# Kernel tuning notes

Hardware: AMD Instinct MI355X
Metric: run time of the kernel (lower is better)

## Reference

```python
import jax, jax.numpy as jnp
import numpy as np

K = 8  # args.k


def setup_inputs() -> dict:
    key = jax.random.key(0)
    k1, k2, k3 = jax.random.split(key, 3)
    b, n_pre, n_cur = 1, 8192, 16384
    pre_xyzs = jax.random.normal(k1, (b, 3, n_pre), dtype=jnp.float32)
    cur_xyzs = jax.random.normal(k2, (b, 3, n_cur), dtype=jnp.float32)
    # UpsampleNumLayer output range: sigmoid * (max_upsample_num - 1) + 1  in [1, 8]
    upsample_num = jax.random.uniform(k3, (b, n_pre), dtype=jnp.float32) * 7.0 + 1.0
    return {"pre_xyzs": pre_xyzs, "cur_xyzs": cur_xyzs, "upsample_num": upsample_num}


def _sqdist(a, b):
    # a: (b, n, 3), b: (b, m, 3) -> (b, n, m) squared euclidean distances
    return ((a * a).sum(-1)[:, :, None]
            + (b * b).sum(-1)[:, None, :]
            - 2.0 * jnp.einsum('bnc,bmc->bnm', a, b))


def reference(pre_xyzs, cur_xyzs, upsample_num):
    # pre_xyzs: (b, 3, n_pre); cur_xyzs: (b, 3, n_cur); upsample_num: (b, n_pre)
    pre_t = pre_xyzs.transpose(0, 2, 1)  # (b, n_pre, 3)
    cur_t = cur_xyzs.transpose(0, 2, 1)  # (b, n_cur, 3)

    # knnquery_heap(1, pre, cur): nearest pre index for each cur point -> (b, n_cur)
    cur2pre = jnp.argmin(_sqdist(cur_t, pre_t), axis=-1)

    # knnquery_heap(K, cur, pre): K nearest cur indices for each pre point -> (b, n_pre, K)
    _, knn_idx = jax.lax.top_k(-_sqdist(pre_t, cur_t), K)

    # real_center: gather cur2pre at knn_idx -> (b, n_pre, K)
    real_center = jax.vmap(lambda c2p, idx: c2p[idx])(cur2pre, knn_idx)
    expect_center = jnp.arange(pre_xyzs.shape[2])[None, :, None]  # (1, n_pre, 1)
    mask = (expect_center == real_center).astype(pre_xyzs.dtype)  # (b, n_pre, K)

    # knn_xyzs: gather cur_xyzs columns at knn_idx -> (b, 3, n_pre, K)
    knn_xyzs = jax.vmap(lambda pts, idx: pts[:, idx])(cur_xyzs, knn_idx)

    diff = knn_xyzs - pre_xyzs[..., None]              # (b, 3, n_pre, K)
    dist = jnp.sqrt((diff * diff).sum(axis=1))         # (b, n_pre, K), L2 over channel dim
    mean_distance = (dist * mask).sum(axis=-1) / upsample_num  # (b, n_pre)
    return mean_distance
```

## Files before the change

kernel.cpp:

```cpp
#include <hip/hip_runtime.h>

#define N_PRE 8192
#define N_CUR 16384
#define KNN   8


#define MAPPED_INF 0xFF800000u

__device__ __forceinline__ unsigned key_of(float d) {
    unsigned b = __float_as_uint(d);
    return b ^ (0x80000000u | (unsigned)((int)b >> 31));
}
__device__ __forceinline__ float float_of_key(unsigned k) {
    unsigned b = (k & 0x80000000u) ? (k ^ 0x80000000u) : ~k;
    return __uint_as_float(b);
}
__device__ __forceinline__ unsigned shfl_u32(unsigned x, int src) {
    return (unsigned)__shfl((int)x, src);
}
__device__ __forceinline__ unsigned shfl_up1_u32(unsigned x) {
    return (unsigned)__shfl_up((int)x, 1);
}

__global__ __launch_bounds__(256) void prep_kernel(
        const float* __restrict__ pre, const float* __restrict__ cur,
        float4* __restrict__ pre4, float4* __restrict__ cur4) {
    int i = blockIdx.x * 256 + threadIdx.x;
    if (i < N_CUR) {
        float x = cur[i], y = cur[N_CUR + i], z = cur[2 * N_CUR + i];
        cur4[i] = make_float4(x, y, z, fmaf(x, x, fmaf(y, y, z * z)));
    }
    if (i < N_PRE) {
        float x = pre[i], y = pre[N_PRE + i], z = pre[2 * N_PRE + i];
        pre4[i] = make_float4(-2.f * x, -2.f * y, -2.f * z,
                              fmaf(x, x, fmaf(y, y, z * z)));
    }
}

#define TILE_A 2048

__global__ __launch_bounds__(1024) void cur2pre_kernel(
        const float4* __restrict__ pre4, const float4* __restrict__ cur4,
        unsigned* __restrict__ c2p) {
    __shared__ float4 sp[TILE_A];
    const int tid  = threadIdx.x;
    const int lane = tid & 63;
    const int w    = tid >> 6;
    const int j0   = blockIdx.x * 64 + w * 4;

    const float4 c0 = cur4[j0 + 0];
    const float4 c1 = cur4[j0 + 1];
    const float4 c2 = cur4[j0 + 2];
    const float4 c3 = cur4[j0 + 3];

    const float INF = __int_as_float(0x7F800000);
    float b0 = INF, b1 = INF, b2 = INF, b3 = INF;
    int   i0 = 0,   i1 = 0,   i2 = 0,   i3 = 0;

    for (int tile = 0; tile < N_PRE; tile += TILE_A) {
        __syncthreads();
        for (int k = tid; k < TILE_A; k += 1024) sp[k] = pre4[tile + k];
        __syncthreads();

#pragma unroll 4
        for (int s = 0; s < TILE_A; s += 64) {
            float4 q = sp[s + lane];
            int idx = tile + s + lane;
            float d0 = fmaf(q.x, c0.x, fmaf(q.y, c0.y, fmaf(q.z, c0.z, q.w)));
            float d1 = fmaf(q.x, c1.x, fmaf(q.y, c1.y, fmaf(q.z, c1.z, q.w)));
            float d2 = fmaf(q.x, c2.x, fmaf(q.y, c2.y, fmaf(q.z, c2.z, q.w)));
            float d3 = fmaf(q.x, c3.x, fmaf(q.y, c3.y, fmaf(q.z, c3.z, q.w)));
            if (d0 < b0) { b0 = d0; i0 = idx; }
            if (d1 < b1) { b1 = d1; i1 = idx; }
            if (d2 < b2) { b2 = d2; i2 = idx; }
            if (d3 < b3) { b3 = d3; i3 = idx; }
        }
    }

    float        bs[4] = {b0, b1, b2, b3};
    int          is[4] = {i0, i1, i2, i3};
#pragma unroll
    for (int t = 0; t < 4; ++t) {
        unsigned long long v =
            (((unsigned long long)key_of(bs[t])) << 32) | (unsigned)is[t];
#pragma unroll
        for (int off = 32; off > 0; off >>= 1) {
            unsigned long long o = __shfl_xor((unsigned long long)v, off);
            v = (o < v) ? o : v;
        }
        if (lane == 0) c2p[j0 + t] = (unsigned)(v & 0xFFFFFFFFull);
    }
}

#define TILE_B 2048

__global__ __launch_bounds__(1024) void knn_finalize_kernel(
        const float4* __restrict__ pre4, const float4* __restrict__ cur4,
        const float* __restrict__ ups,
        const unsigned* __restrict__ c2p,
        float* __restrict__ out) {
    __shared__ float4 sc[TILE_B];
    const int tid  = threadIdx.x;
    const int lane = tid & 63;
    const int w    = tid >> 6;
    const int i0   = blockIdx.x * 32 + w * 2;
    const int i1   = i0 + 1;

    const float4 p0 = pre4[i0];
    const float4 p1 = pre4[i1];

    unsigned ld0 = MAPPED_INF, li0 = 0u;
    unsigned ld1 = MAPPED_INF, li1 = 0u;
    float t80 = __int_as_float(0x7F800000);
    float t81 = t80;

    for (int tile = 0; tile < N_CUR; tile += TILE_B) {
        __syncthreads();
        for (int k = tid; k < TILE_B; k += 1024) sc[k] = cur4[tile + k];
        __syncthreads();

#pragma unroll 4
        for (int s = 0; s < TILE_B; s += 64) {
            float4 c = sc[s + lane];
            float d0 = fmaf(p0.x, c.x, fmaf(p0.y, c.y, fmaf(p0.z, c.z, c.w)));
            float d1 = fmaf(p1.x, c.x, fmaf(p1.y, c.y, fmaf(p1.z, c.z, c.w)));
            int jj = tile + s + lane;

            unsigned long long m0 = __ballot(d0 < t80);
            while (m0) {
                int src = __ffsll(m0) - 1;
                float fd = __uint_as_float(shfl_u32(__float_as_uint(d0), src));
                unsigned kd = key_of(fd);
                unsigned kj = shfl_u32((unsigned)jj, src);
                unsigned ud = shfl_up1_u32(ld0);
                unsigned uj = shfl_up1_u32(li0);
                if (lane == 0) ud = 0u;
                bool hi = kd < ud, lo = kd < ld0;
                ld0 = hi ? ud : (lo ? kd : ld0);
                li0 = hi ? uj : (lo ? kj : li0);
                t80 = float_of_key(shfl_u32(ld0, 7));
                m0 = (m0 & (m0 - 1)) & __ballot(d0 < t80);
            }

            unsigned long long m1 = __ballot(d1 < t81);
            while (m1) {
                int src = __ffsll(m1) - 1;
                float fd = __uint_as_float(shfl_u32(__float_as_uint(d1), src));
                unsigned kd = key_of(fd);
                unsigned kj = shfl_u32((unsigned)jj, src);
                unsigned ud = shfl_up1_u32(ld1);
                unsigned uj = shfl_up1_u32(li1);
                if (lane == 0) ud = 0u;
                bool hi = kd < ud, lo = kd < ld1;
                ld1 = hi ? ud : (lo ? kd : ld1);
                li1 = hi ? uj : (lo ? kj : li1);
                t81 = float_of_key(shfl_u32(ld1, 7));
                m1 = (m1 & (m1 - 1)) & __ballot(d1 < t81);
            }
        }
    }

    unsigned ja = shfl_u32(li0, lane & 7);
    unsigned jb = shfl_u32(li1, lane & 7);
    unsigned j  = (lane < 8) ? ja : jb;

    float contrib = 0.f;
    if (lane < 16) {
        float4 c = cur4[j];
        float px = -0.5f * ((lane < 8) ? p0.x : p1.x);
        float py = -0.5f * ((lane < 8) ? p0.y : p1.y);
        float pz = -0.5f * ((lane < 8) ? p0.z : p1.z);
        float dx = c.x - px, dy = c.y - py, dz = c.z - pz;
        float dsq = fmaf(dx, dx, fmaf(dy, dy, dz * dz));
        unsigned owner = c2p[j];
        unsigned iexp  = (lane < 8) ? (unsigned)i0 : (unsigned)i1;
        contrib = (owner == iexp) ? sqrtf(dsq) : 0.f;
    }
    contrib += __shfl_xor(contrib, 1);
    contrib += __shfl_xor(contrib, 2);
    contrib += __shfl_xor(contrib, 4);
    if (lane == 0) out[i0] = contrib / ups[i0];
    if (lane == 8) out[i1] = contrib / ups[i1];
}

extern "C" void kernel_launch(void* const* d_in, const int* in_sizes, int n_in,
                              void* d_out, int out_size, void* d_ws, size_t ws_size,
                              hipStream_t stream) {
    const float* pre = (const float*)d_in[0];
    const float* cur = (const float*)d_in[1];
    const float* ups = (const float*)d_in[2];
    float* out = (float*)d_out;

    char* ws = (char*)d_ws;
    unsigned* c2p = (unsigned*)ws;
    float4*   pre4 = (float4*)(ws + 65536);
    float4*   cur4 = (float4*)(ws + 65536 + 131072);

    prep_kernel<<<N_CUR / 256, 256, 0, stream>>>(pre, cur, pre4, cur4);

    cur2pre_kernel<<<N_CUR / 64, 1024, 0, stream>>>(pre4, cur4, c2p);

    knn_finalize_kernel<<<N_PRE / 32, 1024, 0, stream>>>(pre4, cur4, ups, c2p, out);
}
```

Measured before the change: 142.8 us.

## Shrink blocks and register-tile more queries per wave in both KNN kernels

Both distance kernels move from 1024-thread to 256-thread blocks. The KNN kernel now keeps four pre points per wave instead of two and loads four candidates per lane per step, so each shared-memory float4 load feeds more distance computations. A wave-wide early-out (__any over per-lane minima against the current thresholds) skips the ballot/insert loops when no candidate can enter any of the four heaps. Smaller blocks mean each block restages the whole point set through shared memory, so global and LDS staging traffic grows; register pressure also rises.

```diff
diff --git a/kernel.cpp b/kernel.cpp
--- a/kernel.cpp
+++ b/kernel.cpp
@@ -39,62 +39,65 @@
 
 #define TILE_A 2048
 
-__global__ __launch_bounds__(1024) void cur2pre_kernel(
+__global__ __launch_bounds__(256, 4) void cur2pre_kernel(
         const float4* __restrict__ pre4, const float4* __restrict__ cur4,
         unsigned* __restrict__ c2p) {
     __shared__ float4 sp[TILE_A];
     const int tid  = threadIdx.x;
     const int lane = tid & 63;
     const int w    = tid >> 6;
-    const int j0   = blockIdx.x * 64 + w * 4;
-
-    const float4 c0 = cur4[j0 + 0];
-    const float4 c1 = cur4[j0 + 1];
-    const float4 c2 = cur4[j0 + 2];
-    const float4 c3 = cur4[j0 + 3];
-
-    const float INF = __int_as_float(0x7F800000);
-    float b0 = INF, b1 = INF, b2 = INF, b3 = INF;
-    int   i0 = 0,   i1 = 0,   i2 = 0,   i3 = 0;
+    const int j0   = blockIdx.x * 16 + w * 4;
+
+    float4 cq[4];
+#pragma unroll
+    for (int q = 0; q < 4; ++q) cq[q] = cur4[j0 + q];
+
+    float    bq[4];
+    unsigned biq[4];
+#pragma unroll
+    for (int q = 0; q < 4; ++q) { bq[q] = __int_as_float(0x7F800000); biq[q] = 0u; }
 
     for (int tile = 0; tile < N_PRE; tile += TILE_A) {
         __syncthreads();
-        for (int k = tid; k < TILE_A; k += 1024) sp[k] = pre4[tile + k];
-        __syncthreads();
-
-#pragma unroll 4
-        for (int s = 0; s < TILE_A; s += 64) {
-            float4 q = sp[s + lane];
-            int idx = tile + s + lane;
-            float d0 = fmaf(q.x, c0.x, fmaf(q.y, c0.y, fmaf(q.z, c0.z, q.w)));
-            float d1 = fmaf(q.x, c1.x, fmaf(q.y, c1.y, fmaf(q.z, c1.z, q.w)));
-            float d2 = fmaf(q.x, c2.x, fmaf(q.y, c2.y, fmaf(q.z, c2.z, q.w)));
-            float d3 = fmaf(q.x, c3.x, fmaf(q.y, c3.y, fmaf(q.z, c3.z, q.w)));
-            if (d0 < b0) { b0 = d0; i0 = idx; }
-            if (d1 < b1) { b1 = d1; i1 = idx; }
-            if (d2 < b2) { b2 = d2; i2 = idx; }
-            if (d3 < b3) { b3 = d3; i3 = idx; }
+        for (int k = tid; k < TILE_A; k += 256) sp[k] = pre4[tile + k];
+        __syncthreads();
+
+        for (int s = 0; s < TILE_A; s += 256) {
+            float4 c0 = sp[s +       lane];
+            float4 c1 = sp[s +  64 + lane];
+            float4 c2 = sp[s + 128 + lane];
+            float4 c3 = sp[s + 192 + lane];
+            unsigned base = (unsigned)(tile + s + lane);
+#pragma unroll
+            for (int q = 0; q < 4; ++q) {
+                float d0 = fmaf(c0.x, cq[q].x, fmaf(c0.y, cq[q].y, fmaf(c0.z, cq[q].z, c0.w)));
+                float d1 = fmaf(c1.x, cq[q].x, fmaf(c1.y, cq[q].y, fmaf(c1.z, cq[q].z, c1.w)));
+                float d2 = fmaf(c2.x, cq[q].x, fmaf(c2.y, cq[q].y, fmaf(c2.z, cq[q].z, c2.w)));
+                float d3 = fmaf(c3.x, cq[q].x, fmaf(c3.y, cq[q].y, fmaf(c3.z, cq[q].z, c3.w)));
+                if (d0 < bq[q]) { bq[q] = d0; biq[q] = base; }
+                if (d1 < bq[q]) { bq[q] = d1; biq[q] = base + 64; }
+                if (d2 < bq[q]) { bq[q] = d2; biq[q] = base + 128; }
+                if (d3 < bq[q]) { bq[q] = d3; biq[q] = base + 192; }
+            }
         }
     }
 
-    float        bs[4] = {b0, b1, b2, b3};
-    int          is[4] = {i0, i1, i2, i3};
-#pragma unroll
-    for (int t = 0; t < 4; ++t) {
+#pragma unroll
+    for (int q = 0; q < 4; ++q) {
         unsigned long long v =
-            (((unsigned long long)key_of(bs[t])) << 32) | (unsigned)is[t];
+            (((unsigned long long)key_of(bq[q])) << 32) | biq[q];
 #pragma unroll
         for (int off = 32; off > 0; off >>= 1) {
             unsigned long long o = __shfl_xor((unsigned long long)v, off);
             v = (o < v) ? o : v;
         }
-        if (lane == 0) c2p[j0 + t] = (unsigned)(v & 0xFFFFFFFFull);
+        if (lane == 0) c2p[j0 + q] = (unsigned)(v & 0xFFFFFFFFull);
     }
 }
 
 #define TILE_B 2048
 
-__global__ __launch_bounds__(1024) void knn_finalize_kernel(
+__global__ __launch_bounds__(256, 2) void knn_finalize_kernel(
         const float4* __restrict__ pre4, const float4* __restrict__ cur4,
         const float* __restrict__ ups,
         const unsigned* __restrict__ c2p,
@@ -103,84 +106,90 @@
     const int tid  = threadIdx.x;
     const int lane = tid & 63;
     const int w    = tid >> 6;
-    const int i0   = blockIdx.x * 32 + w * 2;
-    const int i1   = i0 + 1;
-
-    const float4 p0 = pre4[i0];
-    const float4 p1 = pre4[i1];
-
-    unsigned ld0 = MAPPED_INF, li0 = 0u;
-    unsigned ld1 = MAPPED_INF, li1 = 0u;
-    float t80 = __int_as_float(0x7F800000);
-    float t81 = t80;
+    const int i0   = blockIdx.x * 16 + w * 4;
+
+    float4 pq[4];
+#pragma unroll
+    for (int t = 0; t < 4; ++t) pq[t] = pre4[i0 + t];
+
+    unsigned ld[4], li[4];
+    float    t8[4];
+#pragma unroll
+    for (int t = 0; t < 4; ++t) {
+        ld[t] = MAPPED_INF; li[t] = 0u; t8[t] = __int_as_float(0x7F800000);
+    }
 
     for (int tile = 0; tile < N_CUR; tile += TILE_B) {
         __syncthreads();
-        for (int k = tid; k < TILE_B; k += 1024) sc[k] = cur4[tile + k];
-        __syncthreads();
-
-#pragma unroll 4
-        for (int s = 0; s < TILE_B; s += 64) {
-            float4 c = sc[s + lane];
-            float d0 = fmaf(p0.x, c.x, fmaf(p0.y, c.y, fmaf(p0.z, c.z, c.w)));
-            float d1 = fmaf(p1.x, c.x, fmaf(p1.y, c.y, fmaf(p1.z, c.z, c.w)));
-            int jj = tile + s + lane;
-
-            unsigned long long m0 = __ballot(d0 < t80);
-            while (m0) {
-                int src = __ffsll(m0) - 1;
-                float fd = __uint_as_float(shfl_u32(__float_as_uint(d0), src));
-                unsigned kd = key_of(fd);
-                unsigned kj = shfl_u32((unsigned)jj, src);
-                unsigned ud = shfl_up1_u32(ld0);
-                unsigned uj = shfl_up1_u32(li0);
-                if (lane == 0) ud = 0u;
-                bool hi = kd < ud, lo = kd < ld0;
-                ld0 = hi ? ud : (lo ? kd : ld0);
-                li0 = hi ? uj : (lo ? kj : li0);
-                t80 = float_of_key(shfl_u32(ld0, 7));
-                m0 = (m0 & (m0 - 1)) & __ballot(d0 < t80);
-            }
-
-            unsigned long long m1 = __ballot(d1 < t81);
-            while (m1) {
-                int src = __ffsll(m1) - 1;
-                float fd = __uint_as_float(shfl_u32(__float_as_uint(d1), src));
-                unsigned kd = key_of(fd);
-                unsigned kj = shfl_u32((unsigned)jj, src);
-                unsigned ud = shfl_up1_u32(ld1);
-                unsigned uj = shfl_up1_u32(li1);
-                if (lane == 0) ud = 0u;
-                bool hi = kd < ud, lo = kd < ld1;
-                ld1 = hi ? ud : (lo ? kd : ld1);
-                li1 = hi ? uj : (lo ? kj : li1);
-                t81 = float_of_key(shfl_u32(ld1, 7));
-                m1 = (m1 & (m1 - 1)) & __ballot(d1 < t81);
+        for (int k = tid; k < TILE_B; k += 256) sc[k] = cur4[tile + k];
+        __syncthreads();
+
+        for (int s = 0; s < TILE_B; s += 256) {
+            float4 c0 = sc[s +       lane];
+            float4 c1 = sc[s +  64 + lane];
+            float4 c2 = sc[s + 128 + lane];
+            float4 c3 = sc[s + 192 + lane];
+            float d[4][4];
+#pragma unroll
+            for (int t = 0; t < 4; ++t) {
+                d[t][0] = fmaf(pq[t].x, c0.x, fmaf(pq[t].y, c0.y, fmaf(pq[t].z, c0.z, c0.w)));
+                d[t][1] = fmaf(pq[t].x, c1.x, fmaf(pq[t].y, c1.y, fmaf(pq[t].z, c1.z, c1.w)));
+                d[t][2] = fmaf(pq[t].x, c2.x, fmaf(pq[t].y, c2.y, fmaf(pq[t].z, c2.z, c2.w)));
+                d[t][3] = fmaf(pq[t].x, c3.x, fmaf(pq[t].y, c3.y, fmaf(pq[t].z, c3.z, c3.w)));
+            }
+            bool ev = false;
+#pragma unroll
+            for (int t = 0; t < 4; ++t) {
+                float dm = fminf(fminf(d[t][0], d[t][1]), fminf(d[t][2], d[t][3]));
+                ev = ev || (dm < t8[t]);
+            }
+            if (__any(ev)) {
+                int base = tile + s;
+#pragma unroll
+                for (int t = 0; t < 4; ++t) {
+#pragma unroll
+                    for (int k = 0; k < 4; ++k) {
+                        unsigned long long m = __ballot(d[t][k] < t8[t]);
+                        while (m) {
+                            int src = __ffsll((long long)m) - 1;
+                            float fd = __uint_as_float(
+                                shfl_u32(__float_as_uint(d[t][k]), src));
+                            unsigned kd = key_of(fd);
+                            unsigned kj = (unsigned)(base + 64 * k + src);
+                            unsigned ud = shfl_up1_u32(ld[t]);
+                            unsigned uj = shfl_up1_u32(li[t]);
+                            if (lane == 0) ud = 0u;
+                            bool hi = kd < ud, lo = kd < ld[t];
+                            ld[t] = hi ? ud : (lo ? kd : ld[t]);
+                            li[t] = hi ? uj : (lo ? kj : li[t]);
+                            t8[t] = float_of_key(shfl_u32(ld[t], 7));
+                            m = (m & (m - 1)) & __ballot(d[t][k] < t8[t]);
+                        }
+                    }
+                }
             }
         }
     }
 
-    unsigned ja = shfl_u32(li0, lane & 7);
-    unsigned jb = shfl_u32(li1, lane & 7);
-    unsigned j  = (lane < 8) ? ja : jb;
+    unsigned jt[4];
+#pragma unroll
+    for (int t = 0; t < 4; ++t) jt[t] = shfl_u32(li[t], lane & 7);
+    const int g = lane >> 3;
+    unsigned j = (g == 0) ? jt[0] : (g == 1) ? jt[1] : (g == 2) ? jt[2] : jt[3];
 
     float contrib = 0.f;
-    if (lane < 16) {
+    if (lane < 32) {
         float4 c = cur4[j];
-        float px = -0.5f * ((lane < 8) ? p0.x : p1.x);
-        float py = -0.5f * ((lane < 8) ? p0.y : p1.y);
-        float pz = -0.5f * ((lane < 8) ? p0.z : p1.z);
+        float4 p = (g == 0) ? pq[0] : (g == 1) ? pq[1] : (g == 2) ? pq[2] : pq[3];
+        float px = -0.5f * p.x, py = -0.5f * p.y, pz = -0.5f * p.z;
         float dx = c.x - px, dy = c.y - py, dz = c.z - pz;
         float dsq = fmaf(dx, dx, fmaf(dy, dy, dz * dz));
-        unsigned owner = c2p[j];
-        unsigned iexp  = (lane < 8) ? (unsigned)i0 : (unsigned)i1;
-        contrib = (owner == iexp) ? sqrtf(dsq) : 0.f;
+        contrib = (c2p[j] == (unsigned)(i0 + g)) ? sqrtf(dsq) : 0.f;
     }
     contrib += __shfl_xor(contrib, 1);
     contrib += __shfl_xor(contrib, 2);
     contrib += __shfl_xor(contrib, 4);
-    if (lane == 0) out[i0] = contrib / ups[i0];
-    if (lane == 8) out[i1] = contrib / ups[i1];
+    if (lane < 32 && (lane & 7) == 0) out[i0 + g] = contrib / ups[i0 + g];
 }
 
 extern "C" void kernel_launch(void* const* d_in, const int* in_sizes, int n_in,
@@ -192,13 +201,13 @@
     float* out = (float*)d_out;
 
     char* ws = (char*)d_ws;
-    unsigned* c2p = (unsigned*)ws;
+    unsigned* c2p  = (unsigned*)ws;
     float4*   pre4 = (float4*)(ws + 65536);
     float4*   cur4 = (float4*)(ws + 65536 + 131072);
 
     prep_kernel<<<N_CUR / 256, 256, 0, stream>>>(pre, cur, pre4, cur4);
 
-    cur2pre_kernel<<<N_CUR / 64, 1024, 0, stream>>>(pre4, cur4, c2p);
-
-    knn_finalize_kernel<<<N_PRE / 32, 1024, 0, stream>>>(pre4, cur4, ups, c2p, out);
-}
+    cur2pre_kernel<<<N_CUR / 16, 256, 0, stream>>>(pre4, cur4, c2p);
+
+    knn_finalize_kernel<<<N_PRE / 16, 256, 0, stream>>>(pre4, cur4, ups, c2p, out);
+}
```

New measurement: 163.4 us. 14.5% more time.

## Use wave-uniform ballot thresholds in argmin and batch candidate checks in kNN

Applied to the files above, without the earlier changes.

The cur2pre argmin now keeps one wave-wide best value per query. It uses a ballot against that threshold to skip iterations where no lane improves, and runs a 64-lane shuffle reduction only when some lane does. The kNN kernel processes two 64-point chunks per iteration and computes four ballots up front, so the common no-candidate case costs a single branch. Candidate indices are derived from the ballot bit instead of an extra shuffle. The trade-off is extra shuffle reductions early in the scan, when the thresholds are still loose, and the loss of the explicit unroll pragma.

```diff
diff --git a/kernel.cpp b/kernel.cpp
--- a/kernel.cpp
+++ b/kernel.cpp
@@ -54,41 +54,77 @@
     const float4 c3 = cur4[j0 + 3];
 
     const float INF = __int_as_float(0x7F800000);
-    float b0 = INF, b1 = INF, b2 = INF, b3 = INF;
-    int   i0 = 0,   i1 = 0,   i2 = 0,   i3 = 0;
+    float t0 = INF, t1 = INF, t2 = INF, t3 = INF;
+    unsigned long long bv0 = ~0ull, bv1 = ~0ull, bv2 = ~0ull, bv3 = ~0ull;
 
     for (int tile = 0; tile < N_PRE; tile += TILE_A) {
         __syncthreads();
         for (int k = tid; k < TILE_A; k += 1024) sp[k] = pre4[tile + k];
         __syncthreads();
 
-#pragma unroll 4
         for (int s = 0; s < TILE_A; s += 64) {
-            float4 q = sp[s + lane];
-            int idx = tile + s + lane;
-            float d0 = fmaf(q.x, c0.x, fmaf(q.y, c0.y, fmaf(q.z, c0.z, q.w)));
-            float d1 = fmaf(q.x, c1.x, fmaf(q.y, c1.y, fmaf(q.z, c1.z, q.w)));
-            float d2 = fmaf(q.x, c2.x, fmaf(q.y, c2.y, fmaf(q.z, c2.z, q.w)));
-            float d3 = fmaf(q.x, c3.x, fmaf(q.y, c3.y, fmaf(q.z, c3.z, q.w)));
-            if (d0 < b0) { b0 = d0; i0 = idx; }
-            if (d1 < b1) { b1 = d1; i1 = idx; }
-            if (d2 < b2) { b2 = d2; i2 = idx; }
-            if (d3 < b3) { b3 = d3; i3 = idx; }
+            float4 p = sp[s + lane];
+            unsigned idx = (unsigned)(tile + s + lane);
+            float d0 = fmaf(p.x, c0.x, fmaf(p.y, c0.y, fmaf(p.z, c0.z, p.w)));
+            float d1 = fmaf(p.x, c1.x, fmaf(p.y, c1.y, fmaf(p.z, c1.z, p.w)));
+            float d2 = fmaf(p.x, c2.x, fmaf(p.y, c2.y, fmaf(p.z, c2.z, p.w)));
+            float d3 = fmaf(p.x, c3.x, fmaf(p.y, c3.y, fmaf(p.z, c3.z, p.w)));
+
+            unsigned long long m0 = __ballot(d0 < t0);
+            unsigned long long m1 = __ballot(d1 < t1);
+            unsigned long long m2 = __ballot(d2 < t2);
+            unsigned long long m3 = __ballot(d3 < t3);
+
+            if (m0 | m1 | m2 | m3) {
+                if (m0) {
+                    unsigned long long v =
+                        (((unsigned long long)key_of(d0)) << 32) | idx;
+#pragma unroll
+                    for (int off = 32; off > 0; off >>= 1) {
+                        unsigned long long o = __shfl_xor((unsigned long long)v, off);
+                        v = (o < v) ? o : v;
+                    }
+                    if (v < bv0) { bv0 = v; t0 = float_of_key((unsigned)(bv0 >> 32)); }
+                }
+                if (m1) {
+                    unsigned long long v =
+                        (((unsigned long long)key_of(d1)) << 32) | idx;
+#pragma unroll
+                    for (int off = 32; off > 0; off >>= 1) {
+                        unsigned long long o = __shfl_xor((unsigned long long)v, off);
+                        v = (o < v) ? o : v;
+                    }
+                    if (v < bv1) { bv1 = v; t1 = float_of_key((unsigned)(bv1 >> 32)); }
+                }
+                if (m2) {
+                    unsigned long long v =
+                        (((unsigned long long)key_of(d2)) << 32) | idx;
+#pragma unroll
+                    for (int off = 32; off > 0; off >>= 1) {
+                        unsigned long long o = __shfl_xor((unsigned long long)v, off);
+                        v = (o < v) ? o : v;
+                    }
+                    if (v < bv2) { bv2 = v; t2 = float_of_key((unsigned)(bv2 >> 32)); }
+                }
+                if (m3) {
+                    unsigned long long v =
+                        (((unsigned long long)key_of(d3)) << 32) | idx;
+#pragma unroll
+                    for (int off = 32; off > 0; off >>= 1) {
+                        unsigned long long o = __shfl_xor((unsigned long long)v, off);
+                        v = (o < v) ? o : v;
+                    }
+                    if (v < bv3) { bv3 = v; t3 = float_of_key((unsigned)(bv3 >> 32)); }
+                }
+            }
         }
     }
 
-    float        bs[4] = {b0, b1, b2, b3};
-    int          is[4] = {i0, i1, i2, i3};
-#pragma unroll
-    for (int t = 0; t < 4; ++t) {
-        unsigned long long v =
-            (((unsigned long long)key_of(bs[t])) << 32) | (unsigned)is[t];
-#pragma unroll
-        for (int off = 32; off > 0; off >>= 1) {
-            unsigned long long o = __shfl_xor((unsigned long long)v, off);
-            v = (o < v) ? o : v;
-        }
-        if (lane == 0) c2p[j0 + t] = (unsigned)(v & 0xFFFFFFFFull);
+    if (lane == 0) {
+        c2p[j0 + 0] = (unsigned)(bv0 & 0xFFFFFFFFull);
+        c2p[j0 + 1] = (unsigned)(bv1 & 0xFFFFFFFFull);
+        c2p[j0 + 2] = (unsigned)(bv2 & 0xFFFFFFFFull);
+        c2p[j0 + 3] = (unsigned)(bv3 & 0xFFFFFFFFull);
     }
 }
 
@@ -119,43 +155,77 @@
         for (int k = tid; k < TILE_B; k += 1024) sc[k] = cur4[tile + k];
         __syncthreads();
 
-#pragma unroll 4
-        for (int s = 0; s < TILE_B; s += 64) {
-            float4 c = sc[s + lane];
-            float d0 = fmaf(p0.x, c.x, fmaf(p0.y, c.y, fmaf(p0.z, c.z, c.w)));
-            float d1 = fmaf(p1.x, c.x, fmaf(p1.y, c.y, fmaf(p1.z, c.z, c.w)));
-            int jj = tile + s + lane;
-
-            unsigned long long m0 = __ballot(d0 < t80);
-            while (m0) {
-                int src = __ffsll(m0) - 1;
-                float fd = __uint_as_float(shfl_u32(__float_as_uint(d0), src));
-                unsigned kd = key_of(fd);
-                unsigned kj = shfl_u32((unsigned)jj, src);
-                unsigned ud = shfl_up1_u32(ld0);
-                unsigned uj = shfl_up1_u32(li0);
-                if (lane == 0) ud = 0u;
-                bool hi = kd < ud, lo = kd < ld0;
-                ld0 = hi ? ud : (lo ? kd : ld0);
-                li0 = hi ? uj : (lo ? kj : li0);
-                t80 = float_of_key(shfl_u32(ld0, 7));
-                m0 = (m0 & (m0 - 1)) & __ballot(d0 < t80);
-            }
-
-            unsigned long long m1 = __ballot(d1 < t81);
-            while (m1) {
-                int src = __ffsll(m1) - 1;
-                float fd = __uint_as_float(shfl_u32(__float_as_uint(d1), src));
-                unsigned kd = key_of(fd);
-                unsigned kj = shfl_u32((unsigned)jj, src);
-                unsigned ud = shfl_up1_u32(ld1);
-                unsigned uj = shfl_up1_u32(li1);
-                if (lane == 0) ud = 0u;
-                bool hi = kd < ud, lo = kd < ld1;
-                ld1 = hi ? ud : (lo ? kd : ld1);
-                li1 = hi ? uj : (lo ? kj : li1);
-                t81 = float_of_key(shfl_u32(ld1, 7));
-                m1 = (m1 & (m1 - 1)) & __ballot(d1 < t81);
+        for (int s = 0; s < TILE_B; s += 128) {
+            float4 ca = sc[s + lane];
+            float4 cb = sc[s + 64 + lane];
+            float d0a = fmaf(p0.x, ca.x, fmaf(p0.y, ca.y, fmaf(p0.z, ca.z, ca.w)));
+            float d0b = fmaf(p0.x, cb.x, fmaf(p0.y, cb.y, fmaf(p0.z, cb.z, cb.w)));
+            float d1a = fmaf(p1.x, ca.x, fmaf(p1.y, ca.y, fmaf(p1.z, ca.z, ca.w)));
+            float d1b = fmaf(p1.x, cb.x, fmaf(p1.y, cb.y, fmaf(p1.z, cb.z, cb.w)));
+
+            unsigned long long m0a = __ballot(d0a < t80);
+            unsigned long long m0b = __ballot(d0b < t80);
+            unsigned long long m1a = __ballot(d1a < t81);
+            unsigned long long m1b = __ballot(d1b < t81);
+
+            if (m0a | m0b | m1a | m1b) {
+                int base = tile + s;
+                while (m0a) {
+                    int src = __ffsll((long long)m0a) - 1;
+                    unsigned kd = key_of(__uint_as_float(
+                        shfl_u32(__float_as_uint(d0a), src)));
+                    unsigned kj = (unsigned)(base + src);
+                    unsigned ud = shfl_up1_u32(ld0);
+                    unsigned uj = shfl_up1_u32(li0);
+                    if (lane == 0) ud = 0u;
+                    bool hi = kd < ud, lo = kd < ld0;
+                    ld0 = hi ? ud : (lo ? kd : ld0);
+                    li0 = hi ? uj : (lo ? kj : li0);
+                    t80 = float_of_key(shfl_u32(ld0, 7));
+                    m0a = (m0a & (m0a - 1)) & __ballot(d0a < t80);
+                }
+                while (m0b) {
+                    int src = __ffsll((long long)m0b) - 1;
+                    unsigned kd = key_of(__uint_as_float(
+                        shfl_u32(__float_as_uint(d0b), src)));
+                    unsigned kj = (unsigned)(base + 64 + src);
+                    unsigned ud = shfl_up1_u32(ld0);
+                    unsigned uj = shfl_up1_u32(li0);
+                    if (lane == 0) ud = 0u;
+                    bool hi = kd < ud, lo = kd < ld0;
+                    ld0 = hi ? ud : (lo ? kd : ld0);
+                    li0 = hi ? uj : (lo ? kj : li0);
+                    t80 = float_of_key(shfl_u32(ld0, 7));
+                    m0b = (m0b & (m0b - 1)) & __ballot(d0b < t80);
+                }
+                while (m1a) {
+                    int src = __ffsll((long long)m1a) - 1;
+                    unsigned kd = key_of(__uint_as_float(
+                        shfl_u32(__float_as_uint(d1a), src)));
+                    unsigned kj = (unsigned)(base + src);
+                    unsigned ud = shfl_up1_u32(ld1);
+                    unsigned uj = shfl_up1_u32(li1);
+                    if (lane == 0) ud = 0u;
+                    bool hi = kd < ud, lo = kd < ld1;
+                    ld1 = hi ? ud : (lo ? kd : ld1);
+                    li1 = hi ? uj : (lo ? kj : li1);
+                    t81 = float_of_key(shfl_u32(ld1, 7));
+                    m1a = (m1a & (m1a - 1)) & __ballot(d1a < t81);
+                }
+                while (m1b) {
+                    int src = __ffsll((long long)m1b) - 1;
+                    unsigned kd = key_of(__uint_as_float(
+                        shfl_u32(__float_as_uint(d1b), src)));
+                    unsigned kj = (unsigned)(base + 64 + src);
+                    unsigned ud = shfl_up1_u32(ld1);
+                    unsigned uj = shfl_up1_u32(li1);
+                    if (lane == 0) ud = 0u;
+                    bool hi = kd < ud, lo = kd < ld1;
+                    ld1 = hi ? ud : (lo ? kd : ld1);
+                    li1 = hi ? uj : (lo ? kj : li1);
+                    t81 = float_of_key(shfl_u32(ld1, 7));
+                    m1b = (m1b & (m1b - 1)) & __ballot(d1b < t81);
+                }
             }
         }
     }
@@ -192,7 +262,7 @@
     float* out = (float*)d_out;
 
     char* ws = (char*)d_ws;
-    unsigned* c2p = (unsigned*)ws;
+    unsigned* c2p  = (unsigned*)ws;
     float4*   pre4 = (float4*)(ws + 65536);
     float4*   cur4 = (float4*)(ws + 65536 + 131072);
 
```

Result: slower. 149.5 us (+4.7%).
